# Kernel tuning notes

Hardware: AMD Instinct MI355X
Metric: run time of the kernel (lower is better)

Reference implementation:

```python
import jax, jax.numpy as jnp
import numpy as np

B, L, D_MODEL, D_FF, N_EXPERTS, TOP_K = 32, 256, 512, 2048, 8, 2
EPS = 1e-9


def setup_inputs() -> dict:
    key = jax.random.key(0)
    ks = jax.random.split(key, 7)
    scale1 = 1.0 / np.sqrt(D_MODEL)
    scale2 = 1.0 / np.sqrt(D_FF)
    return {
        "cycle_curve_data": jax.random.normal(ks[0], (B, L, D_MODEL), jnp.float32),
        "logits": jax.random.normal(ks[1], (B, N_EXPERTS), jnp.float32),
        "moe_masks": jax.random.randint(ks[2], (B, N_EXPERTS), 0, 2, jnp.int32),
        "W1": jax.random.normal(ks[3], (N_EXPERTS, D_MODEL, D_FF), jnp.float32) * scale1,
        "b1": jax.random.normal(ks[4], (N_EXPERTS, D_FF), jnp.float32) * scale1,
        "W2": jax.random.normal(ks[5], (N_EXPERTS, D_FF, D_MODEL), jnp.float32) * scale2,
        "b2": jax.random.normal(ks[6], (N_EXPERTS, D_MODEL), jnp.float32) * scale2,
    }


def _gates(logits, moe_masks):
    # softmax over experts, zero out unavailable experts, keep top-k, renormalize
    mask = (moe_masks == 1).astype(logits.dtype)               # [B, E]
    p = jax.nn.softmax(logits, axis=1) * mask                  # [B, E]
    _, idx = jax.lax.top_k(p, TOP_K)                           # [B, K]
    topk_mask = jnp.zeros_like(p).at[jnp.arange(p.shape[0])[:, None], idx].set(1.0)
    p = p * topk_mask
    return p / (jnp.sum(p, axis=1, keepdims=True) + EPS)       # [B, E]


def reference(cycle_curve_data, logits, moe_masks, W1, b1, W2, b2):
    gates = _gates(logits, moe_masks)                          # [B, E]
    x = cycle_curve_data                                       # [B, L, D]
    # dense equivalent of per-expert gather -> MLP -> gate-weighted scatter-combine
    h = jnp.einsum("bld,edf->eblf", x, W1) + b1[:, None, None, :]   # [E,B,L,F]
    h = jax.nn.gelu(h, approximate=False)
    out = jnp.einsum("be,eblf,efd->bld", gates, h, W2)
    out = out + jnp.einsum("be,ed->bd", gates, b2)[:, None, :]      # [B,L,D]
    return out
```

## Files before the change

kernel.cpp:

```cpp
#include <hip/hip_runtime.h>

#define B_SZ 32
#define L_SZ 256
#define D_SZ 512
#define F_SZ 2048
#define E_SZ 8
#define P_SZ 64
#define BK2  32

typedef __attribute__((ext_vector_type(8)))  short bf16x8;
typedef __attribute__((ext_vector_type(16))) float f32x16;

__device__ __forceinline__ unsigned short f2bf(float f) {
  unsigned int u = __builtin_bit_cast(unsigned int, f);
  u += 0x7fffu + ((u >> 16) & 1u);
  return (unsigned short)(u >> 16);
}

__device__ __forceinline__ void async16(const void* g, void* l) {
  __builtin_amdgcn_global_load_lds(
      (const __attribute__((address_space(1))) unsigned int*)g,
      (__attribute__((address_space(3))) unsigned int*)l, 16, 0, 0);
}

__device__ __forceinline__ float gelu_f(float x) {
  float a = fabsf(x) * 0.70710678118654752f;
  float t = __builtin_amdgcn_rcpf(1.0f + 0.3275911f * a);
  float y = t * (0.254829592f +
            t * (-0.284496736f +
            t * (1.421413741f +
            t * (-1.453152027f +
            t * 1.061405429f))));
  float e = __expf(-a * a);
  float erf_abs = 1.0f - y * e;
  float erf_v = (x < 0.f) ? -erf_abs : erf_abs;
  return 0.5f * x * (1.0f + erf_v);
}

__device__ __forceinline__ void transpose_tile(
    const float* __restrict__ ip, unsigned short* __restrict__ op,
    int R, int C, int r0, int c0, float* tile, int tid) {
  int tx = tid & 63, ty = tid >> 6;
#pragma unroll
  for (int i = 0; i < 16; ++i) {
    int r = i * 4 + ty;
    tile[r * 65 + tx] = ip[(size_t)(r0 + r) * C + c0 + tx];
  }
  __syncthreads();
#pragma unroll
  for (int uu = 0; uu < 4; ++uu) {
    int u = uu * 256 + tid;
    int cc = u >> 4, q = u & 15;
    ushort4 o;
    o.x = f2bf(tile[(q * 4 + 0) * 65 + cc]);
    o.y = f2bf(tile[(q * 4 + 1) * 65 + cc]);
    o.z = f2bf(tile[(q * 4 + 2) * 65 + cc]);
    o.w = f2bf(tile[(q * 4 + 3) * 65 + cc]);
    *(ushort4*)(op + (size_t)(c0 + cc) * R + r0 + q * 4) = o;
  }
}

#define PREP_CONV_BLKS 4096
#define PREP_TR_BLKS   2048
#define PREP_TOTAL     (1 + PREP_CONV_BLKS + PREP_TR_BLKS)

__global__ __launch_bounds__(256) void prep_kernel(
    const float* __restrict__ logits, const int* __restrict__ masks,
    const float* __restrict__ x,
    const float* __restrict__ W1,
    int* __restrict__ sel_e, float* __restrict__ sel_g,
    unsigned short* __restrict__ xb,
    unsigned short* __restrict__ w1t) {
  __shared__ float tile[64 * 65];
  int blk = blockIdx.x;
  int tid = threadIdx.x;

  if (blk == 0) {
    int b = tid;
    if (b >= B_SZ) return;
    float lg[E_SZ], p[E_SZ];
    float mx = -1e30f;
    for (int e = 0; e < E_SZ; ++e) { lg[e] = logits[b * E_SZ + e]; mx = fmaxf(mx, lg[e]); }
    float s = 0.f;
    for (int e = 0; e < E_SZ; ++e) { p[e] = expf(lg[e] - mx); s += p[e]; }
    for (int e = 0; e < E_SZ; ++e) p[e] = (masks[b * E_SZ + e] == 1) ? (p[e] / s) : 0.f;
    int i0 = 0, i1 = 1; float v0 = -1.f, v1 = -1.f;
    for (int e = 0; e < E_SZ; ++e) {
      float v = p[e];
      if (v > v0)      { v1 = v0; i1 = i0; v0 = v; i0 = e; }
      else if (v > v1) { v1 = v;  i1 = e; }
    }
    float den = v0 + v1 + 1e-9f;
    sel_e[2 * b] = i0;  sel_e[2 * b + 1] = i1;
    sel_g[2 * b] = v0 / den;
    sel_g[2 * b + 1] = v1 / den;
    return;
  }
  blk -= 1;

  if (blk < PREP_CONV_BLKS) {
    int i = blk * 256 + tid;
    float4 v = ((const float4*)x)[i];
    ushort4 o;
    o.x = f2bf(v.x); o.y = f2bf(v.y); o.z = f2bf(v.z); o.w = f2bf(v.w);
    ((ushort4*)xb)[i] = o;
    return;
  }
  blk -= PREP_CONV_BLKS;

  int z = blk >> 8;
  int rem = blk & 255;
  int tr = rem >> 5, tc = rem & 31;
  transpose_tile(W1 + (size_t)z * D_SZ * F_SZ, w1t + (size_t)z * D_SZ * F_SZ,
                 D_SZ, F_SZ, tr * 64, tc * 64, tile, tid);
}

__global__ __launch_bounds__(256, 4) void moe_gemm1(
    const unsigned short* __restrict__ Xb,
    const unsigned short* __restrict__ W1t,
    const float* __restrict__ b1,
    const int* __restrict__ sel_e,
    unsigned short* __restrict__ H,
    const float* __restrict__ W2,
    unsigned short* __restrict__ w2t) {
  __shared__ __align__(16) char smem[32768];
  int tid = threadIdx.x;
  int lin = blockIdx.x;

  if (lin >= 2048) {
    int blk = lin - 2048;
    int z = blk >> 8;
    int rem = blk & 255;
    int tr = rem >> 3, tc = rem & 7;
    transpose_tile(W2 + (size_t)z * F_SZ * D_SZ, w2t + (size_t)z * F_SZ * D_SZ,
                   F_SZ, D_SZ, tr * 64, tc * 64, (float*)smem, tid);
    return;
  }

  unsigned short* As = (unsigned short*)smem;
  unsigned short* Bs = (unsigned short*)(smem + 16384);

  int f  = lin & 15;
  int l0 = ((lin >> 4) & 1) * 128;
  int p  = lin >> 5;
  int f0 = f * 128;
  int b  = p >> 1;
  int e  = sel_e[p];

  int lane = tid & 63;
  int w = tid >> 6, wm = w & 1, wn = w >> 1;
  int m32 = lane & 31, kh = lane >> 5;
  int sw = (m32 >> 1) & 3;

  const unsigned short* Abase = Xb  + ((size_t)b * L_SZ + l0) * D_SZ;
  const unsigned short* Bbase = W1t + ((size_t)e * F_SZ + f0) * D_SZ;

  int seg0 = w * 128 + lane;
  int row0 = seg0 >> 2, ks0 = ((seg0 & 3) ^ ((row0 >> 1) & 3)) * 8;
  int seg1 = seg0 + 64;
  int row1 = seg1 >> 2, ks1 = ((seg1 & 3) ^ ((row1 >> 1) & 3)) * 8;

  const size_t aoff0 = (size_t)row0 * D_SZ + ks0;
  const size_t aoff1 = (size_t)row1 * D_SZ + ks1;

  f32x16 acc[2][2] = {};

#define G1_COMPUTE(CB)                                                       \
  _Pragma("unroll")                                                          \
  for (int s = 0; s < 2; ++s) {                                              \
    int ko = ((((s << 1) | kh) ^ sw) << 3) + (CB) * 4096;                    \
    bf16x8 a0  = *(const bf16x8*)&As[(wm * 64 +      m32) * BK2 + ko];       \
    bf16x8 a1  = *(const bf16x8*)&As[(wm * 64 + 32 + m32) * BK2 + ko];       \
    bf16x8 b0  = *(const bf16x8*)&Bs[(wn * 64 +      m32) * BK2 + ko];       \
    bf16x8 b1f = *(const bf16x8*)&Bs[(wn * 64 + 32 + m32) * BK2 + ko];       \
    acc[0][0] = __builtin_amdgcn_mfma_f32_32x32x16_bf16(a0, b0,  acc[0][0], 0, 0, 0); \
    acc[0][1] = __builtin_amdgcn_mfma_f32_32x32x16_bf16(a0, b1f, acc[0][1], 0, 0, 0); \
    acc[1][0] = __builtin_amdgcn_mfma_f32_32x32x16_bf16(a1, b0,  acc[1][0], 0, 0, 0); \
    acc[1][1] = __builtin_amdgcn_mfma_f32_32x32x16_bf16(a1, b1f, acc[1][1], 0, 0, 0); \
  }

  async16(Abase + aoff0, &As[seg0 * 8]);
  async16(Abase + aoff1, &As[seg1 * 8]);
  async16(Bbase + aoff0, &Bs[seg0 * 8]);
  async16(Bbase + aoff1, &Bs[seg1 * 8]);
  __syncthreads();

#pragma unroll 2
  for (int t = 0; t < 15; ++t) {
    int cb = t & 1, nb = cb ^ 1;
    int kk = (t + 1) * BK2;
    async16(Abase + aoff0 + kk, &As[(nb * 512 + seg0) * 8]);
    async16(Abase + aoff1 + kk, &As[(nb * 512 + seg1) * 8]);
    async16(Bbase + aoff0 + kk, &Bs[(nb * 512 + seg0) * 8]);
    async16(Bbase + aoff1 + kk, &Bs[(nb * 512 + seg1) * 8]);
    G1_COMPUTE(cb)
    __syncthreads();
  }
  G1_COMPUTE(1)
#undef G1_COMPUTE

  float b1v[2];
#pragma unroll
  for (int tj = 0; tj < 2; ++tj)
    b1v[tj] = b1[e * F_SZ + f0 + wn * 64 + tj * 32 + m32];

  unsigned short* Hp = H + ((size_t)p * L_SZ + l0) * F_SZ + f0;
#pragma unroll
  for (int ti = 0; ti < 2; ++ti)
#pragma unroll
    for (int tj = 0; tj < 2; ++tj) {
      int col = wn * 64 + tj * 32 + m32;
#pragma unroll
      for (int r = 0; r < 16; ++r) {
        int row = wm * 64 + ti * 32 + (r & 3) + 8 * (r >> 2) + 4 * kh;
        Hp[(size_t)row * F_SZ + col] = f2bf(gelu_f(acc[ti][tj][r] + b1v[tj]));
      }
    }
}

__global__ __launch_bounds__(256, 4) void moe_gemm2(
    const unsigned short* __restrict__ H,
    const unsigned short* __restrict__ W2t,
    const float* __restrict__ b2,
    const int* __restrict__ sel_e,
    const float* __restrict__ sel_g,
    float* __restrict__ part,
    float* __restrict__ Out) {
  __shared__ __align__(16) unsigned short As[2][512 * 8];
  __shared__ __align__(16) unsigned short Bs[2][512 * 8];

  int lin = blockIdx.x;
  int q   = lin & 7;
  int d   = (lin >> 3) & 3;
  int g8  = lin >> 5;
  int gg  = g8 * 8 + q;
  int p   = gg >> 1;
  int l0  = (gg & 1) * 128;
  int d0  = d * 128;
  int b   = p >> 1;
  int e   = sel_e[p];
  float g = sel_g[p];

  int tid = threadIdx.x;
  int lane = tid & 63;
  int w = tid >> 6, wm = w & 1, wn = w >> 1;
  int m32 = lane & 31, kh = lane >> 5;
  int sw = (m32 >> 1) & 3;

  const unsigned short* Abase = H   + ((size_t)p * L_SZ + l0) * F_SZ;
  const unsigned short* Bbase = W2t + ((size_t)e * D_SZ + d0) * F_SZ;

  int seg0 = w * 128 + lane;
  int row0 = seg0 >> 2, ks0 = ((seg0 & 3) ^ ((row0 >> 1) & 3)) * 8;
  int seg1 = seg0 + 64;
  int row1 = seg1 >> 2, ks1 = ((seg1 & 3) ^ ((row1 >> 1) & 3)) * 8;

  const size_t aoff0 = (size_t)row0 * F_SZ + ks0;
  const size_t aoff1 = (size_t)row1 * F_SZ + ks1;

  f32x16 acc[2][2] = {};

#define G2_COMPUTE(CB)                                                       \
  _Pragma("unroll")                                                          \
  for (int s = 0; s < 2; ++s) {                                              \
    int ko = ((((s << 1) | kh) ^ sw) << 3);                                  \
    bf16x8 a0  = *(const bf16x8*)&As[CB][(wm * 64 +      m32) * BK2 + ko];   \
    bf16x8 a1  = *(const bf16x8*)&As[CB][(wm * 64 + 32 + m32) * BK2 + ko];   \
    bf16x8 b0  = *(const bf16x8*)&Bs[CB][(wn * 64 +      m32) * BK2 + ko];   \
    bf16x8 b1f = *(const bf16x8*)&Bs[CB][(wn * 64 + 32 + m32) * BK2 + ko];   \
    acc[0][0] = __builtin_amdgcn_mfma_f32_32x32x16_bf16(a0, b0,  acc[0][0], 0, 0, 0); \
    acc[0][1] = __builtin_amdgcn_mfma_f32_32x32x16_bf16(a0, b1f, acc[0][1], 0, 0, 0); \
    acc[1][0] = __builtin_amdgcn_mfma_f32_32x32x16_bf16(a1, b0,  acc[1][0], 0, 0, 0); \
    acc[1][1] = __builtin_amdgcn_mfma_f32_32x32x16_bf16(a1, b1f, acc[1][1], 0, 0, 0); \
  }

  async16(Abase + aoff0, &As[0][seg0 * 8]);
  async16(Abase + aoff1, &As[0][seg1 * 8]);
  async16(Bbase + aoff0, &Bs[0][seg0 * 8]);
  async16(Bbase + aoff1, &Bs[0][seg1 * 8]);
  __syncthreads();

#pragma unroll 2
  for (int t = 0; t < 63; ++t) {
    int cb = t & 1, nb = cb ^ 1;
    int kk = (t + 1) * BK2;
    async16(Abase + aoff0 + kk, &As[nb][seg0 * 8]);
    async16(Abase + aoff1 + kk, &As[nb][seg1 * 8]);
    async16(Bbase + aoff0 + kk, &Bs[nb][seg0 * 8]);
    async16(Bbase + aoff1 + kk, &Bs[nb][seg1 * 8]);
    G2_COMPUTE(cb)
    __syncthreads();
  }
  G2_COMPUTE(1)
#undef G2_COMPUTE

  float bias[2] = {0.f, 0.f};
  if (p & 1) {
    int e0 = sel_e[2 * b], e1 = sel_e[2 * b + 1];
    float g0 = sel_g[2 * b], g1 = sel_g[2 * b + 1];
#pragma unroll
    for (int tj = 0; tj < 2; ++tj) {
      int dd = d0 + wn * 64 + tj * 32 + m32;
      bias[tj] = g0 * b2[e0 * D_SZ + dd] + g1 * b2[e1 * D_SZ + dd];
    }
  }
  float* dst = (p & 1) ? Out : part;
  float* Op = dst + ((size_t)b * L_SZ + l0) * D_SZ + d0;
#pragma unroll
  for (int ti = 0; ti < 2; ++ti)
#pragma unroll
    for (int tj = 0; tj < 2; ++tj) {
      int col = wn * 64 + tj * 32 + m32;
#pragma unroll
      for (int r = 0; r < 16; ++r) {
        int row = wm * 64 + ti * 32 + (r & 3) + 8 * (r >> 2) + 4 * kh;
        Op[(size_t)row * D_SZ + col] = g * acc[ti][tj][r] + bias[tj];
      }
    }
}

__global__ __launch_bounds__(256) void combine_kernel(
    const float* __restrict__ part, float* __restrict__ Out) {
  int i = blockIdx.x * 256 + threadIdx.x;
  float4 pv = ((const float4*)part)[i];
  float4 o  = ((float4*)Out)[i];
  o.x += pv.x; o.y += pv.y; o.z += pv.z; o.w += pv.w;
  ((float4*)Out)[i] = o;
}

extern "C" void kernel_launch(void* const* d_in, const int* in_sizes, int n_in,
                              void* d_out, int out_size, void* d_ws, size_t ws_size,
                              hipStream_t stream) {
  const float* x      = (const float*)d_in[0];
  const float* logits = (const float*)d_in[1];
  const int*   masks  = (const int*)d_in[2];
  const float* W1     = (const float*)d_in[3];
  const float* b1     = (const float*)d_in[4];
  const float* W2     = (const float*)d_in[5];
  const float* b2     = (const float*)d_in[6];
  float* out = (float*)d_out;

  char* ws = (char*)d_ws;
  int*   sel_e = (int*)ws;
  float* sel_g = (float*)(ws + 256);
  unsigned short* xb  = (unsigned short*)(ws + 1024);
  unsigned short* w1t = xb  + (size_t)B_SZ * L_SZ * D_SZ;
  unsigned short* w2t = w1t + (size_t)E_SZ * F_SZ * D_SZ;
  unsigned short* Hbuf = w2t + (size_t)E_SZ * D_SZ * F_SZ;
  float* part = (float*)(ws + 1024);

  prep_kernel<<<PREP_TOTAL, 256, 0, stream>>>(logits, masks, x, W1,
                                              sel_e, sel_g, xb, w1t);
  moe_gemm1<<<4096, 256, 0, stream>>>(xb, w1t, b1, sel_e, Hbuf, W2, w2t);
  moe_gemm2<<<512, 256, 0, stream>>>(Hbuf, w2t, b2, sel_e, sel_g, part, out);
  combine_kernel<<<(B_SZ * L_SZ * D_SZ / 4) / 256, 256, 0, stream>>>(part, out);
}
```

Before: 242.1 us.

## Widen gemm1 tiles to 128x256 with 512 threads and double gemm2 K-step

gemm1 now runs 512-thread blocks that each compute a 128x256 output tile, so every X tile loaded into LDS is reused across twice as many F columns. This halves the number of gemm1 blocks, and the W2 transpose blocks are respread over 512 threads. gemm2 now stages 64 K elements per barrier, as two 32-wide halves, which halves the number of syncs per block. The cost is more LDS per block (48KB for gemm1), which may lower occupancy. The gemm1 epilogue indexing relies on wn covering 4 wave columns, and it is not clear whether it was updated to match.

```diff
diff --git a/kernel.cpp b/kernel.cpp
--- a/kernel.cpp
+++ b/kernel.cpp
@@ -37,19 +37,21 @@
   return 0.5f * x * (1.0f + erf_v);
 }
 
+template <int NT>
 __device__ __forceinline__ void transpose_tile(
     const float* __restrict__ ip, unsigned short* __restrict__ op,
     int R, int C, int r0, int c0, float* tile, int tid) {
   int tx = tid & 63, ty = tid >> 6;
-#pragma unroll
-  for (int i = 0; i < 16; ++i) {
-    int r = i * 4 + ty;
+  constexpr int RY = NT / 64;
+#pragma unroll
+  for (int i = 0; i < 64 / RY; ++i) {
+    int r = i * RY + ty;
     tile[r * 65 + tx] = ip[(size_t)(r0 + r) * C + c0 + tx];
   }
   __syncthreads();
 #pragma unroll
-  for (int uu = 0; uu < 4; ++uu) {
-    int u = uu * 256 + tid;
+  for (int uu = 0; uu < 1024 / NT; ++uu) {
+    int u = uu * NT + tid;
     int cc = u >> 4, q = u & 15;
     ushort4 o;
     o.x = f2bf(tile[(q * 4 + 0) * 65 + cc]);
@@ -111,11 +113,11 @@
   int z = blk >> 8;
   int rem = blk & 255;
   int tr = rem >> 5, tc = rem & 31;
-  transpose_tile(W1 + (size_t)z * D_SZ * F_SZ, w1t + (size_t)z * D_SZ * F_SZ,
-                 D_SZ, F_SZ, tr * 64, tc * 64, tile, tid);
-}
-
-__global__ __launch_bounds__(256, 4) void moe_gemm1(
+  transpose_tile<256>(W1 + (size_t)z * D_SZ * F_SZ, w1t + (size_t)z * D_SZ * F_SZ,
+                      D_SZ, F_SZ, tr * 64, tc * 64, tile, tid);
+}
+
+__global__ __launch_bounds__(512, 4) void moe_gemm1(
     const unsigned short* __restrict__ Xb,
     const unsigned short* __restrict__ W1t,
     const float* __restrict__ b1,
@@ -123,76 +125,75 @@
     unsigned short* __restrict__ H,
     const float* __restrict__ W2,
     unsigned short* __restrict__ w2t) {
-  __shared__ __align__(16) char smem[32768];
+  __shared__ __align__(16) char smem[49152];
   int tid = threadIdx.x;
   int lin = blockIdx.x;
 
-  if (lin >= 2048) {
-    int blk = lin - 2048;
+  if (lin >= 1024) {
+    int blk = lin - 1024;
     int z = blk >> 8;
     int rem = blk & 255;
     int tr = rem >> 3, tc = rem & 7;
-    transpose_tile(W2 + (size_t)z * F_SZ * D_SZ, w2t + (size_t)z * F_SZ * D_SZ,
-                   F_SZ, D_SZ, tr * 64, tc * 64, (float*)smem, tid);
+    transpose_tile<512>(W2 + (size_t)z * F_SZ * D_SZ, w2t + (size_t)z * F_SZ * D_SZ,
+                        F_SZ, D_SZ, tr * 64, tc * 64, (float*)smem, tid);
     return;
   }
 
   unsigned short* As = (unsigned short*)smem;
   unsigned short* Bs = (unsigned short*)(smem + 16384);
 
-  int f  = lin & 15;
-  int l0 = ((lin >> 4) & 1) * 128;
-  int p  = lin >> 5;
-  int f0 = f * 128;
+  int f  = lin & 7;
+  int l0 = ((lin >> 3) & 1) * 128;
+  int p  = lin >> 4;
+  int f0 = f * 256;
   int b  = p >> 1;
   int e  = sel_e[p];
 
   int lane = tid & 63;
-  int w = tid >> 6, wm = w & 1, wn = w >> 1;
+  int w = tid >> 6;
+  int wm = w & 1, wn = w >> 1;
   int m32 = lane & 31, kh = lane >> 5;
   int sw = (m32 >> 1) & 3;
 
   const unsigned short* Abase = Xb  + ((size_t)b * L_SZ + l0) * D_SZ;
   const unsigned short* Bbase = W1t + ((size_t)e * F_SZ + f0) * D_SZ;
 
-  int seg0 = w * 128 + lane;
-  int row0 = seg0 >> 2, ks0 = ((seg0 & 3) ^ ((row0 >> 1) & 3)) * 8;
-  int seg1 = seg0 + 64;
-  int row1 = seg1 >> 2, ks1 = ((seg1 & 3) ^ ((row1 >> 1) & 3)) * 8;
-
-  const size_t aoff0 = (size_t)row0 * D_SZ + ks0;
-  const size_t aoff1 = (size_t)row1 * D_SZ + ks1;
+  int sa   = tid;
+  int rowa = sa >> 2,  ka  = ((sa  & 3) ^ ((rowa >> 1) & 3)) * 8;
+  int sb1  = tid + 512;
+  int rowb = sb1 >> 2, kb1 = ((sb1 & 3) ^ ((rowb >> 1) & 3)) * 8;
+
+  const size_t aoffA  = (size_t)rowa * D_SZ + ka;
+  const size_t aoffB1 = (size_t)rowb * D_SZ + kb1;
 
   f32x16 acc[2][2] = {};
 
 #define G1_COMPUTE(CB)                                                       \
   _Pragma("unroll")                                                          \
   for (int s = 0; s < 2; ++s) {                                              \
-    int ko = ((((s << 1) | kh) ^ sw) << 3) + (CB) * 4096;                    \
-    bf16x8 a0  = *(const bf16x8*)&As[(wm * 64 +      m32) * BK2 + ko];       \
-    bf16x8 a1  = *(const bf16x8*)&As[(wm * 64 + 32 + m32) * BK2 + ko];       \
-    bf16x8 b0  = *(const bf16x8*)&Bs[(wn * 64 +      m32) * BK2 + ko];       \
-    bf16x8 b1f = *(const bf16x8*)&Bs[(wn * 64 + 32 + m32) * BK2 + ko];       \
+    int ko = ((((s << 1) | kh) ^ sw) << 3);                                  \
+    bf16x8 a0  = *(const bf16x8*)&As[(CB) * 4096 + (wm * 64 +      m32) * BK2 + ko]; \
+    bf16x8 a1  = *(const bf16x8*)&As[(CB) * 4096 + (wm * 64 + 32 + m32) * BK2 + ko]; \
+    bf16x8 b0  = *(const bf16x8*)&Bs[(CB) * 8192 + (wn * 64 +      m32) * BK2 + ko]; \
+    bf16x8 b1f = *(const bf16x8*)&Bs[(CB) * 8192 + (wn * 64 + 32 + m32) * BK2 + ko]; \
     acc[0][0] = __builtin_amdgcn_mfma_f32_32x32x16_bf16(a0, b0,  acc[0][0], 0, 0, 0); \
     acc[0][1] = __builtin_amdgcn_mfma_f32_32x32x16_bf16(a0, b1f, acc[0][1], 0, 0, 0); \
     acc[1][0] = __builtin_amdgcn_mfma_f32_32x32x16_bf16(a1, b0,  acc[1][0], 0, 0, 0); \
     acc[1][1] = __builtin_amdgcn_mfma_f32_32x32x16_bf16(a1, b1f, acc[1][1], 0, 0, 0); \
   }
 
-  async16(Abase + aoff0, &As[seg0 * 8]);
-  async16(Abase + aoff1, &As[seg1 * 8]);
-  async16(Bbase + aoff0, &Bs[seg0 * 8]);
-  async16(Bbase + aoff1, &Bs[seg1 * 8]);
+  async16(Abase + aoffA,  &As[sa * 8]);
+  async16(Bbase + aoffA,  &Bs[sa * 8]);
+  async16(Bbase + aoffB1, &Bs[sb1 * 8]);
   __syncthreads();
 
 #pragma unroll 2
   for (int t = 0; t < 15; ++t) {
     int cb = t & 1, nb = cb ^ 1;
     int kk = (t + 1) * BK2;
-    async16(Abase + aoff0 + kk, &As[(nb * 512 + seg0) * 8]);
-    async16(Abase + aoff1 + kk, &As[(nb * 512 + seg1) * 8]);
-    async16(Bbase + aoff0 + kk, &Bs[(nb * 512 + seg0) * 8]);
-    async16(Bbase + aoff1 + kk, &Bs[(nb * 512 + seg1) * 8]);
+    async16(Abase + aoffA  + kk, &As[nb * 4096 + sa * 8]);
+    async16(Bbase + aoffA  + kk, &Bs[nb * 8192 + sa * 8]);
+    async16(Bbase + aoffB1 + kk, &Bs[nb * 8192 + sb1 * 8]);
     G1_COMPUTE(cb)
     __syncthreads();
   }
@@ -226,8 +227,8 @@
     const float* __restrict__ sel_g,
     float* __restrict__ part,
     float* __restrict__ Out) {
-  __shared__ __align__(16) unsigned short As[2][512 * 8];
-  __shared__ __align__(16) unsigned short Bs[2][512 * 8];
+  __shared__ __align__(16) unsigned short As[2][2][128 * BK2];
+  __shared__ __align__(16) unsigned short Bs[2][2][128 * BK2];
 
   int lin = blockIdx.x;
   int q   = lin & 7;
@@ -260,39 +261,47 @@
 
   f32x16 acc[2][2] = {};
 
+#define G2_STAGE(NB, T) do {                                                 \
+    size_t kk = (size_t)(T) * 64;                                            \
+    async16(Abase + aoff0 + kk,      &As[NB][0][seg0 * 8]);                  \
+    async16(Abase + aoff1 + kk,      &As[NB][0][seg1 * 8]);                  \
+    async16(Bbase + aoff0 + kk,      &Bs[NB][0][seg0 * 8]);                  \
+    async16(Bbase + aoff1 + kk,      &Bs[NB][0][seg1 * 8]);                  \
+    async16(Abase + aoff0 + kk + 32, &As[NB][1][seg0 * 8]);                  \
+    async16(Abase + aoff1 + kk + 32, &As[NB][1][seg1 * 8]);                  \
+    async16(Bbase + aoff0 + kk + 32, &Bs[NB][1][seg0 * 8]);                  \
+    async16(Bbase + aoff1 + kk + 32, &Bs[NB][1][seg1 * 8]);                  \
+  } while (0)
+
 #define G2_COMPUTE(CB)                                                       \
   _Pragma("unroll")                                                          \
+  for (int h = 0; h < 2; ++h)                                                \
+  _Pragma("unroll")                                                          \
   for (int s = 0; s < 2; ++s) {                                              \
-    int ko = ((((s << 1) | kh) ^ sw) << 3);                                  \
-    bf16x8 a0  = *(const bf16x8*)&As[CB][(wm * 64 +      m32) * BK2 + ko];   \
-    bf16x8 a1  = *(const bf16x8*)&As[CB][(wm * 64 + 32 + m32) * BK2 + ko];   \
-    bf16x8 b0  = *(const bf16x8*)&Bs[CB][(wn * 64 +      m32) * BK2 + ko];   \
-    bf16x8 b1f = *(const bf16x8*)&Bs[CB][(wn * 64 + 32 + m32) * BK2 + ko];   \
+    int ko = (((s << 1) | kh) ^ sw) << 3;                                    \
+    bf16x8 a0  = *(const bf16x8*)&As[CB][h][(wm * 64 +      m32) * BK2 + ko]; \
+    bf16x8 a1  = *(const bf16x8*)&As[CB][h][(wm * 64 + 32 + m32) * BK2 + ko]; \
+    bf16x8 b0  = *(const bf16x8*)&Bs[CB][h][(wn * 64 +      m32) * BK2 + ko]; \
+    bf16x8 b1f = *(const bf16x8*)&Bs[CB][h][(wn * 64 + 32 + m32) * BK2 + ko]; \
     acc[0][0] = __builtin_amdgcn_mfma_f32_32x32x16_bf16(a0, b0,  acc[0][0], 0, 0, 0); \
     acc[0][1] = __builtin_amdgcn_mfma_f32_32x32x16_bf16(a0, b1f, acc[0][1], 0, 0, 0); \
     acc[1][0] = __builtin_amdgcn_mfma_f32_32x32x16_bf16(a1, b0,  acc[1][0], 0, 0, 0); \
     acc[1][1] = __builtin_amdgcn_mfma_f32_32x32x16_bf16(a1, b1f, acc[1][1], 0, 0, 0); \
   }
 
-  async16(Abase + aoff0, &As[0][seg0 * 8]);
-  async16(Abase + aoff1, &As[0][seg1 * 8]);
-  async16(Bbase + aoff0, &Bs[0][seg0 * 8]);
-  async16(Bbase + aoff1, &Bs[0][seg1 * 8]);
+  G2_STAGE(0, 0);
   __syncthreads();
 
 #pragma unroll 2
-  for (int t = 0; t < 63; ++t) {
+  for (int t = 0; t < 31; ++t) {
     int cb = t & 1, nb = cb ^ 1;
-    int kk = (t + 1) * BK2;
-    async16(Abase + aoff0 + kk, &As[nb][seg0 * 8]);
-    async16(Abase + aoff1 + kk, &As[nb][seg1 * 8]);
-    async16(Bbase + aoff0 + kk, &Bs[nb][seg0 * 8]);
-    async16(Bbase + aoff1 + kk, &Bs[nb][seg1 * 8]);
+    G2_STAGE(nb, t + 1);
     G2_COMPUTE(cb)
     __syncthreads();
   }
   G2_COMPUTE(1)
 #undef G2_COMPUTE
+#undef G2_STAGE
 
   float bias[2] = {0.f, 0.f};
   if (p & 1) {
@@ -351,7 +360,7 @@
 
   prep_kernel<<<PREP_TOTAL, 256, 0, stream>>>(logits, masks, x, W1,
                                               sel_e, sel_g, xb, w1t);
-  moe_gemm1<<<4096, 256, 0, stream>>>(xb, w1t, b1, sel_e, Hbuf, W2, w2t);
+  moe_gemm1<<<3072, 512, 0, stream>>>(xb, w1t, b1, sel_e, Hbuf, W2, w2t);
   moe_gemm2<<<512, 256, 0, stream>>>(Hbuf, w2t, b2, sel_e, sel_g, part, out);
   combine_kernel<<<(B_SZ * L_SZ * D_SZ / 4) / 256, 256, 0, stream>>>(part, out);
 }
```

New measurement: 248.2 us. 2.5% more time.
